# Optimization experiments

Measured on AMD Instinct MI355X. Metric: run time of the kernel, lower is better.

## Reference

```python
import jax, jax.numpy as jnp
import numpy as np

N, E, F_IN, H, C, G, NC = 10000, 160000, 512, 8, 64, 64, 64


def setup_inputs() -> dict:
    key = jax.random.key(0)
    ks = jax.random.split(key, 16)
    d = {}
    d['x'] = jax.random.normal(ks[0], (N, F_IN), jnp.float32)
    d['edge_index'] = jax.random.randint(ks[1], (2, E), 0, N, dtype=jnp.int32)
    d['batch'] = jnp.sort(jax.random.randint(ks[2], (N,), 0, G, dtype=jnp.int32))
    s = 0.05
    d['enc_W'] = jax.random.normal(ks[3], (F_IN, H * C), jnp.float32) * s
    d['enc_b'] = jnp.zeros((H * C,), jnp.float32)
    d['W1'] = jax.random.normal(ks[4], (H * C, H * C), jnp.float32) * s
    d['as1'] = jax.random.normal(ks[5], (H, C), jnp.float32) * s
    d['ad1'] = jax.random.normal(ks[6], (H, C), jnp.float32) * s
    d['b1'] = jnp.zeros((H * C,), jnp.float32)
    d['g1'] = jnp.ones((H * C,), jnp.float32)
    d['be1'] = jnp.zeros((H * C,), jnp.float32)
    d['W2'] = jax.random.normal(ks[7], (H * C, H * C), jnp.float32) * s
    d['as2'] = jax.random.normal(ks[8], (H, C), jnp.float32) * s
    d['ad2'] = jax.random.normal(ks[9], (H, C), jnp.float32) * s
    d['b2'] = jnp.zeros((H * C,), jnp.float32)
    d['g2'] = jnp.ones((H * C,), jnp.float32)
    d['be2'] = jnp.zeros((H * C,), jnp.float32)
    d['W3'] = jax.random.normal(ks[10], (H * C, C), jnp.float32) * s
    d['as3'] = jax.random.normal(ks[11], (1, C), jnp.float32) * s
    d['ad3'] = jax.random.normal(ks[12], (1, C), jnp.float32) * s
    d['b3'] = jnp.zeros((C,), jnp.float32)
    d['g3'] = jnp.ones((C,), jnp.float32)
    d['be3'] = jnp.zeros((C,), jnp.float32)
    d['lin_W'] = jax.random.normal(ks[13], (C, NC), jnp.float32) * s
    d['lin_b'] = jnp.zeros((NC,), jnp.float32)
    return d


def _gat_conv(x, src, dst, W, a_s, a_d, bias, concat):
    # PyG GATConv (eval mode, self-loops already appended to src/dst)
    n = x.shape[0]
    heads, c = a_s.shape
    h = (x @ W).reshape(n, heads, c)                      # [N,H,C]
    logits = (h * a_s).sum(-1)[src] + (h * a_d).sum(-1)[dst]  # [E',H]
    logits = jax.nn.leaky_relu(logits, 0.2)
    m = jax.ops.segment_max(logits, dst, num_segments=n)  # segment softmax over dst
    e = jnp.exp(logits - m[dst])
    s = jax.ops.segment_sum(e, dst, num_segments=n)
    alpha = e / (s[dst] + 1e-16)                          # [E',H]
    out = jax.ops.segment_sum(alpha[:, :, None] * h[src], dst, num_segments=n)
    out = out.reshape(n, heads * c) if concat else out.mean(axis=1)
    return out + bias


def _bn(x, g, b):
    # BatchNorm1d, training-mode statistics (biased var), eps=1e-5
    mu = x.mean(axis=0)
    var = ((x - mu) ** 2).mean(axis=0)
    return g * (x - mu) / jnp.sqrt(var + 1e-5) + b


def reference(x, edge_index, batch, enc_W, enc_b,
              W1, as1, ad1, b1, g1, be1,
              W2, as2, ad2, b2, g2, be2,
              W3, as3, ad3, b3, g3, be3,
              lin_W, lin_b):
    n = x.shape[0]
    loops = jnp.arange(n, dtype=edge_index.dtype)
    src = jnp.concatenate([edge_index[0], loops])
    dst = jnp.concatenate([edge_index[1], loops])
    x = x @ enc_W + enc_b
    # layer 1 (concat heads) + bn + elu + residual
    h = x
    x = _gat_conv(x, src, dst, W1, as1, ad1, b1, True)
    x = jax.nn.elu(_bn(x, g1, be1))
    x = h + x
    # layer 2
    h = x
    x = _gat_conv(x, src, dst, W2, as2, ad2, b2, True)
    x = jax.nn.elu(_bn(x, g2, be2))
    x = h + x
    # layer 3 (heads=1, mean/no-concat), bn, no elu, no residual (shape mismatch)
    x = _gat_conv(x, src, dst, W3, as3, ad3, b3, False)
    x = _bn(x, g3, be3)
    # global mean pool over graphs
    sums = jax.ops.segment_sum(x, batch, num_segments=G)
    cnt = jax.ops.segment_sum(jnp.ones((n,), x.dtype), batch, num_segments=G)
    xg = sums / jnp.clip(cnt, 1.0)[:, None]
    return xg @ lin_W + lin_b
```

## Files before the change

### kernel.cpp

```cpp
#include <hip/hip_runtime.h>
#include <hip/hip_bf16.h>
#include <math.h>

#define NNODES 10000
#define RPAD   10240
#define MPAD   10112
#define EDGES  160000
#define EPLUS  170000
#define FIN    512
#define HEADS8 8
#define CH     64
#define HC     512
#define NG     64
#define NCLS   64
#define NSTAT  256
#define NSTAT3 64

typedef _Float16 f16x8 __attribute__((ext_vector_type(8)));
typedef _Float16 f16x4 __attribute__((ext_vector_type(4)));
typedef _Float16 f16x2 __attribute__((ext_vector_type(2)));
typedef float    f32x4 __attribute__((ext_vector_type(4)));

#define GLD_LDS16(g, l)                                                        \
    __builtin_amdgcn_global_load_lds(                                          \
        (const __attribute__((address_space(1))) void*)(g),                    \
        (__attribute__((address_space(3))) void*)(l), 16, 0, 0)

#define PREP_CNT  665
#define PREP_CONV 5000
__global__ void prep_all(const int* __restrict__ ei, int* __restrict__ deg,
                         const int* __restrict__ batch, int* __restrict__ goff,
                         const float* __restrict__ x_in, _Float16* __restrict__ x16,
                         const float* __restrict__ Wa, const float* __restrict__ Wb,
                         const float* __restrict__ Wc, const float* __restrict__ Wd,
                         _Float16* __restrict__ Ta, _Float16* __restrict__ Tb,
                         _Float16* __restrict__ Tc, _Float16* __restrict__ Td,
                         _Float16* __restrict__ g16pad, float* __restrict__ g3opad)
{
    const int b   = blockIdx.x;
    const int tid = threadIdx.x;
    if (b < PREP_CNT) {
        const float4 z4 = make_float4(0.f, 0.f, 0.f, 0.f);
        if (b < 60)
            ((float4*)g16pad)[b * 256 + tid] = z4;
        else if (b < 75)
            ((float4*)g3opad)[(b - 60) * 256 + tid] = z4;
        int e = b * 256 + tid;
        if (e < NNODES) {
            int bb = batch[e];
            int bprev = (e == 0) ? -1 : batch[e - 1];
            for (int g = bprev + 1; g <= bb; ++g) goff[g] = e;
            if (e == NNODES - 1)
                for (int g = bb + 1; g <= NG; ++g) goff[g] = NNODES;
        }
        if (e >= EPLUS) return;
        int dst = (e < EDGES) ? ei[EDGES + e] : (e - EDGES);
        atomicAdd(&deg[dst], 1);
    } else if (b < PREP_CNT + PREP_CONV) {
        int i = (b - PREP_CNT) * 256 + tid;
        float4 v = ((const float4*)x_in)[i];
        f16x4 o;
        o[0] = (_Float16)v.x; o[1] = (_Float16)v.y;
        o[2] = (_Float16)v.z; o[3] = (_Float16)v.w;
        ((f16x4*)x16)[i] = o;
    } else {
        int tb = b - (PREP_CNT + PREP_CONV);
        int z  = tb >> 8;
        int rem = tb & 255;
        int bxi = rem & 15, byi = rem >> 4;
        if (z == 3 && bxi >= 2) return;
        const float* W = (z == 0) ? Wa : (z == 1) ? Wb : (z == 2) ? Wc : Wd;
        _Float16*    T = (z == 0) ? Ta : (z == 1) ? Tb : (z == 2) ? Tc : Td;
        const int ldW = (z == 3) ? 64 : 512;
        __shared__ float t[32][33];
        int bx = bxi * 32, by = byi * 32;
        int tx = tid & 31, ty = tid >> 5;
        #pragma unroll
        for (int i = 0; i < 32; i += 8)
            t[ty + i][tx] = W[(size_t)(by + ty + i) * ldW + bx + tx];
        __syncthreads();
        #pragma unroll
        for (int i = 0; i < 32; i += 8)
            T[(size_t)(bx + ty + i) * 512 + by + tx] = (_Float16)t[tx][ty + i];
    }
}

__device__ void exscan_dev(const int* __restrict__ deg, int* __restrict__ off,
                           int* __restrict__ cursor, int* partial )
{
    const int tid = threadIdx.x;
    const int chunk = (NNODES + 255) / 256;
    int begin = tid * chunk;
    int end   = begin + chunk; if (end > NNODES) end = NNODES;
    if (begin > NNODES) begin = NNODES;
    int s = 0;
    for (int i = begin; i < end; ++i) s += deg[i];
    partial[tid] = s;
    __syncthreads();
    for (int o = 1; o < 256; o <<= 1) {
        int v = (tid >= o) ? partial[tid - o] : 0;
        __syncthreads();
        partial[tid] += v;
        __syncthreads();
    }
    int run = (tid > 0) ? partial[tid - 1] : 0;
    for (int i = begin; i < end; ++i) {
        off[i] = run; cursor[i] = run; run += deg[i];
    }
    if (tid == 255) off[NNODES] = run;
}

__global__ __launch_bounds__(256) void gemm_f16_mfma(
    const _Float16* __restrict__ A16, const _Float16* __restrict__ Bt16,
    const float* __restrict__ bias, _Float16* __restrict__ C16,
    float* __restrict__ ssrc, float* __restrict__ sdst,
    const float* __restrict__ a_s, const float* __restrict__ a_d,
    int Mt, int Nn, int K,
    int tail, const int* __restrict__ tp0, int* __restrict__ tp1,
    int* __restrict__ tp2)
{
    __shared__ _Float16 As[128 * 32] __attribute__((aligned(16)));
    __shared__ _Float16 Bs[128 * 32] __attribute__((aligned(16)));
    const int tid  = threadIdx.x;
    const int ncols = Nn >> 7;
    const int nb    = ncols * (Mt >> 7);
    const int bid   = blockIdx.x;

    if (bid >= nb) {
        if (tail == 1) {
            exscan_dev(tp0, tp1, tp2, (int*)As);
        } else if (tail == 2) {
            int e = (bid - nb) * 256 + tid;
            if (e < EPLUS) {
                int srcN, dstN;
                if (e < EDGES) { srcN = tp0[e]; dstN = tp0[EDGES + e]; }
                else           { srcN = dstN = e - EDGES; }
                int pos = atomicAdd(&tp1[dstN], 1);
                tp2[pos] = srcN;
            }
        }
        return;
    }

    const int bt   = bid % ncols;
    const int row0 = (bid / ncols) * 128;
    const int col0 = bt * 128;
    const int wave = tid >> 6;
    const int lane = tid & 63;
    const int wy = wave >> 1, wx = wave & 1;

    const int lrow = lane >> 2;
    const int lk   = (lane & 3) * 8;

    f32x4 acc[4][4] = {};

    for (int k0 = 0; k0 < K; k0 += 32) {
        if (k0) __syncthreads();
        #pragma unroll
        for (int r = 0; r < 2; ++r) {
            const int chunk = r * 4 + wave;
            const int trow  = chunk * 16 + lrow;
            GLD_LDS16(A16 + (size_t)(row0 + trow) * K + k0 + lk,
                      &As[chunk * 512]);
            GLD_LDS16(Bt16 + (size_t)(col0 + trow) * K + k0 + lk,
                      &Bs[chunk * 512]);
        }
        __syncthreads();

        const int quad = lane >> 4;
        const int l16  = lane & 15;
        f16x8 af[4], bf[4];
        #pragma unroll
        for (int m = 0; m < 4; ++m)
            af[m] = *(const f16x8*)&As[(wy * 64 + m * 16 + l16) * 32 + quad * 8];
        #pragma unroll
        for (int n = 0; n < 4; ++n)
            bf[n] = *(const f16x8*)&Bs[(wx * 64 + n * 16 + l16) * 32 + quad * 8];
        #pragma unroll
        for (int m = 0; m < 4; ++m)
            #pragma unroll
            for (int n = 0; n < 4; ++n)
                acc[m][n] = __builtin_amdgcn_mfma_f32_16x16x32_f16(
                    af[m], bf[n], acc[m][n], 0, 0, 0);
    }

    const int quad = lane >> 4;
    const int l16  = lane & 15;
    #pragma unroll
    for (int m = 0; m < 4; ++m) {
        #pragma unroll
        for (int n = 0; n < 4; ++n) {
            const int col = col0 + wx * 64 + n * 16 + l16;
            const float bv = bias ? bias[col] : 0.0f;
            #pragma unroll
            for (int r = 0; r < 4; ++r) {
                const int row = row0 + wy * 64 + m * 16 + quad * 4 + r;
                C16[(size_t)row * Nn + col] = (_Float16)(acc[m][n][r] + bv);
            }
        }
    }

    if (ssrc) {
        const int head = bt * 2 + wx;
        float a_sv[4], a_dv[4];
        #pragma unroll
        for (int n = 0; n < 4; ++n) {
            const int col = col0 + wx * 64 + n * 16 + l16;
            a_sv[n] = a_s[col & 511];
            a_dv[n] = a_d[col & 511];
        }
        #pragma unroll
        for (int m = 0; m < 4; ++m) {
            #pragma unroll
            for (int r = 0; r < 4; ++r) {
                float vs = acc[m][0][r] * a_sv[0] + acc[m][1][r] * a_sv[1]
                         + acc[m][2][r] * a_sv[2] + acc[m][3][r] * a_sv[3];
                float vd = acc[m][0][r] * a_dv[0] + acc[m][1][r] * a_dv[1]
                         + acc[m][2][r] * a_dv[2] + acc[m][3][r] * a_dv[3];
                vs += __shfl_xor(vs, 1); vs += __shfl_xor(vs, 2);
                vs += __shfl_xor(vs, 4); vs += __shfl_xor(vs, 8);
                vd += __shfl_xor(vd, 1); vd += __shfl_xor(vd, 2);
                vd += __shfl_xor(vd, 4); vd += __shfl_xor(vd, 8);
                if (l16 == 0) {
                    const int row = row0 + wy * 64 + m * 16 + quad * 4 + r;
                    ssrc[(size_t)row * HEADS8 + head] = vs;
                    sdst[(size_t)row * HEADS8 + head] = vd;
                }
            }
        }
    }
}

__global__ __launch_bounds__(256) void gemm_f16_mfma_n64(
    const _Float16* __restrict__ A16, const _Float16* __restrict__ Bt16,
    _Float16* __restrict__ C16,
    float* __restrict__ ssrc, float* __restrict__ sdst,
    const float* __restrict__ a_s, const float* __restrict__ a_d)
{
    __shared__ _Float16 As[64 * 32] __attribute__((aligned(16)));
    __shared__ _Float16 Bs[64 * 32] __attribute__((aligned(16)));
    __shared__ float sS[2][64];
    __shared__ float sD[2][64];
    const int tid  = threadIdx.x;
    const int wave = tid >> 6;
    const int lane = tid & 63;
    const int row0 = blockIdx.x * 64;
    const int wy = wave >> 1, wx = wave & 1;

    const int lrow = lane >> 2;
    const int lk   = (lane & 3) * 8;

    f32x4 acc[2][2] = {};

    for (int k0 = 0; k0 < 512; k0 += 32) {
        if (k0) __syncthreads();
        {
            const int trow = wave * 16 + lrow;
            GLD_LDS16(A16 + (size_t)(row0 + trow) * 512 + k0 + lk, &As[wave * 512]);
            GLD_LDS16(Bt16 + (size_t)trow * 512 + k0 + lk, &Bs[wave * 512]);
        }
        __syncthreads();

        const int quad = lane >> 4;
        const int l16  = lane & 15;
        f16x8 af[2], bf[2];
        #pragma unroll
        for (int m = 0; m < 2; ++m)
            af[m] = *(const f16x8*)&As[(wy * 32 + m * 16 + l16) * 32 + quad * 8];
        #pragma unroll
        for (int n = 0; n < 2; ++n)
            bf[n] = *(const f16x8*)&Bs[(wx * 32 + n * 16 + l16) * 32 + quad * 8];
        #pragma unroll
        for (int m = 0; m < 2; ++m)
            #pragma unroll
            for (int n = 0; n < 2; ++n)
                acc[m][n] = __builtin_amdgcn_mfma_f32_16x16x32_f16(
                    af[m], bf[n], acc[m][n], 0, 0, 0);
    }

    const int quad = lane >> 4;
    const int l16  = lane & 15;
    #pragma unroll
    for (int m = 0; m < 2; ++m)
        #pragma unroll
        for (int n = 0; n < 2; ++n) {
            const int col = wx * 32 + n * 16 + l16;
            #pragma unroll
            for (int r = 0; r < 4; ++r) {
                const int row = row0 + wy * 32 + m * 16 + quad * 4 + r;
                C16[(size_t)row * 64 + col] = (_Float16)acc[m][n][r];
            }
        }

    {
        float a_sv[2], a_dv[2];
        #pragma unroll
        for (int n = 0; n < 2; ++n) {
            const int col = wx * 32 + n * 16 + l16;
            a_sv[n] = a_s[col];
            a_dv[n] = a_d[col];
        }
        #pragma unroll
        for (int m = 0; m < 2; ++m)
            #pragma unroll
            for (int r = 0; r < 4; ++r) {
                float vs = acc[m][0][r] * a_sv[0] + acc[m][1][r] * a_sv[1];
                float vd = acc[m][0][r] * a_dv[0] + acc[m][1][r] * a_dv[1];
                vs += __shfl_xor(vs, 1); vs += __shfl_xor(vs, 2);
                vs += __shfl_xor(vs, 4); vs += __shfl_xor(vs, 8);
                vd += __shfl_xor(vd, 1); vd += __shfl_xor(vd, 2);
                vd += __shfl_xor(vd, 4); vd += __shfl_xor(vd, 8);
                if (l16 == 0) {
                    const int lr = wy * 32 + m * 16 + quad * 4 + r;
                    sS[wx][lr] = vs;
                    sD[wx][lr] = vd;
                }
            }
        __syncthreads();
        if (wx == 0 && l16 == 0) {
            #pragma unroll
            for (int m = 0; m < 2; ++m)
                #pragma unroll
                for (int r = 0; r < 4; ++r) {
                    const int lr = wy * 32 + m * 16 + quad * 4 + r;
                    const int row = row0 + lr;
                    ssrc[row] = sS[0][lr] + sS[1][lr];
                    sdst[row] = sD[0][lr] + sD[1][lr];
                }
        }
    }
}

__global__ __launch_bounds__(64) void gat_aggregate8(
    const _Float16* __restrict__ Hf, const float* __restrict__ ssrc,
    const float* __restrict__ sdst, const int* __restrict__ off,
    const int* __restrict__ csr, const float* __restrict__ bias,
    _Float16* __restrict__ out)
{
    const int n    = blockIdx.x;
    const int lane = threadIdx.x;
    const int head = lane >> 3;
    const int e0 = off[n], e1 = off[n + 1];

    float4 sd0 = ((const float4*)(sdst + n * 8))[0];
    float4 sd1 = ((const float4*)(sdst + n * 8))[1];
    float sd[8] = {sd0.x, sd0.y, sd0.z, sd0.w, sd1.x, sd1.y, sd1.z, sd1.w};

    __shared__ float exL[64 * 8];
    __shared__ int   srcL[64];
    float acc[8]  = {};
    float ssum[8] = {};
    for (int base = e0; base < e1; base += 64) {
        int cnt = e1 - base; if (cnt > 64) cnt = 64;
        if (lane < cnt) {
            int s = csr[base + lane];
            srcL[lane] = s;
            float4 s0 = ((const float4*)(ssrc + s * 8))[0];
            float4 s1 = ((const float4*)(ssrc + s * 8))[1];
            float lv[8] = {s0.x, s0.y, s0.z, s0.w, s1.x, s1.y, s1.z, s1.w};
            #pragma unroll
            for (int h = 0; h < 8; ++h) {
                float l = lv[h] + sd[h];
                l = (l > 0.f) ? l : 0.2f * l;
                float ex = __expf(l);
                exL[lane * 8 + h] = ex;
                ssum[h] += ex;
            }
        }
        __syncthreads();
        int j = 0;
        for (; j + 8 <= cnt; j += 8) {
            f16x8 hv[8];
            #pragma unroll
            for (int u = 0; u < 8; ++u)
                hv[u] = *(const f16x8*)(Hf + (size_t)srcL[j + u] * HC + lane * 8);
            #pragma unroll
            for (int u = 0; u < 8; ++u) {
                const float a = exL[(j + u) * 8 + head];
                #pragma unroll
                for (int c = 0; c < 8; ++c)
                    acc[c] = fmaf(a, (float)hv[u][c], acc[c]);
            }
        }
        for (; j + 4 <= cnt; j += 4) {
            const int s0 = srcL[j],     s1 = srcL[j + 1];
            const int s2 = srcL[j + 2], s3 = srcL[j + 3];
            f16x8 h0 = *(const f16x8*)(Hf + (size_t)s0 * HC + lane * 8);
            f16x8 h1 = *(const f16x8*)(Hf + (size_t)s1 * HC + lane * 8);
            f16x8 h2 = *(const f16x8*)(Hf + (size_t)s2 * HC + lane * 8);
            f16x8 h3 = *(const f16x8*)(Hf + (size_t)s3 * HC + lane * 8);
            const float a0 = exL[(j)     * 8 + head];
            const float a1 = exL[(j + 1) * 8 + head];
            const float a2 = exL[(j + 2) * 8 + head];
            const float a3 = exL[(j + 3) * 8 + head];
            #pragma unroll
            for (int c = 0; c < 8; ++c) {
                acc[c] = fmaf(a0, (float)h0[c], acc[c]);
                acc[c] = fmaf(a1, (float)h1[c], acc[c]);
                acc[c] = fmaf(a2, (float)h2[c], acc[c]);
                acc[c] = fmaf(a3, (float)h3[c], acc[c]);
            }
        }
        for (; j < cnt; ++j) {
            const int s = srcL[j];
            f16x8 hv = *(const f16x8*)(Hf + (size_t)s * HC + lane * 8);
            const float al = exL[j * 8 + head];
            #pragma unroll
            for (int c = 0; c < 8; ++c)
                acc[c] = fmaf(al, (float)hv[c], acc[c]);
        }
        __syncthreads();
    }
    #pragma unroll
    for (int h = 0; h < 8; ++h)
        #pragma unroll
        for (int o = 1; o < 64; o <<= 1)
            ssum[h] += __shfl_xor(ssum[h], o);

    const float inv = 1.0f / (ssum[head] + 1e-16f);
    const float* bp = bias + lane * 8;
    f16x8 ov;
    #pragma unroll
    for (int c = 0; c < 8; ++c)
        ov[c] = (_Float16)(acc[c] * inv + bp[c]);
    *(f16x8*)(out + (size_t)n * HC + lane * 8) = ov;
}

__global__ __launch_bounds__(64) void gat_aggregate1(
    const _Float16* __restrict__ Hf, const float* __restrict__ ssrc,
    const float* __restrict__ sdst, const int* __restrict__ off,
    const int* __restrict__ csr, const float* __restrict__ bias,
    float* __restrict__ out)
{
    const int n    = blockIdx.x;
    const int lane = threadIdx.x;
    const int e0 = off[n], e1 = off[n + 1];
    const float sd = sdst[n];

    __shared__ float exL[64];
    __shared__ int   srcL[64];
    float acc = 0.f, ssum = 0.f;
    for (int base = e0; base < e1; base += 64) {
        int cnt = e1 - base; if (cnt > 64) cnt = 64;
        if (lane < cnt) {
            int s = csr[base + lane];
            srcL[lane] = s;
            float l = ssrc[s] + sd;
            l = (l > 0.f) ? l : 0.2f * l;
            float ex = __expf(l);
            exL[lane] = ex;
            ssum += ex;
        }
        __syncthreads();
        int j = 0;
        for (; j + 4 <= cnt; j += 4) {
            const int s0 = srcL[j],     s1 = srcL[j + 1];
            const int s2 = srcL[j + 2], s3 = srcL[j + 3];
            float h0 = (float)Hf[(size_t)s0 * 64 + lane];
            float h1 = (float)Hf[(size_t)s1 * 64 + lane];
            float h2 = (float)Hf[(size_t)s2 * 64 + lane];
            float h3 = (float)Hf[(size_t)s3 * 64 + lane];
            acc = fmaf(exL[j],     h0, acc);
            acc = fmaf(exL[j + 1], h1, acc);
            acc = fmaf(exL[j + 2], h2, acc);
            acc = fmaf(exL[j + 3], h3, acc);
        }
        for (; j < cnt; ++j)
            acc = fmaf(exL[j], (float)Hf[(size_t)srcL[j] * 64 + lane], acc);
        __syncthreads();
    }
    #pragma unroll
    for (int o = 1; o < 64; o <<= 1)
        ssum += __shfl_xor(ssum, o);

    out[(size_t)n * 64 + lane] = acc / (ssum + 1e-16f) + bias[lane];
}

__global__ __launch_bounds__(256) void bn_stats_f16(
    const _Float16* __restrict__ x,
    float* __restrict__ psum, float* __restrict__ psq)
{
    const int t    = threadIdx.x;
    const int lane = t & 63;
    const int wv   = t >> 6;
    const int w    = blockIdx.x * 4 + wv;
    float s[8] = {}, q[8] = {};
    #pragma unroll
    for (int k = 0; k < RPAD / 2048; ++k) {
        const int r0 = w + k * 2048;
        f16x8 v0 = *(const f16x8*)(x + (size_t)r0 * HC + lane * 8);
        f16x8 v1 = *(const f16x8*)(x + (size_t)(r0 + 1024) * HC + lane * 8);
        #pragma unroll
        for (int j = 0; j < 8; ++j) {
            float f0 = (float)v0[j], f1 = (float)v1[j];
            s[j] += f0 + f1;
            q[j] += f0 * f0 + f1 * f1;
        }
    }
    __shared__ float ls[4][HC];
    __shared__ float lq[4][HC];
    #pragma unroll
    for (int j = 0; j < 8; ++j) {
        ls[wv][lane * 8 + j] = s[j];
        lq[wv][lane * 8 + j] = q[j];
    }
    __syncthreads();
    const size_t bo = (size_t)blockIdx.x * HC;
    #pragma unroll
    for (int k = 0; k < 2; ++k) {
        const int ch = t + k * 256;
        psum[bo + ch] = ls[0][ch] + ls[1][ch] + ls[2][ch] + ls[3][ch];
        psq [bo + ch] = lq[0][ch] + lq[1][ch] + lq[2][ch] + lq[3][ch];
    }
}

__global__ __launch_bounds__(256) void bn_stats3(
    const float* __restrict__ x,
    float* __restrict__ psum, float* __restrict__ psq)
{
    const int t    = threadIdx.x;
    const int c4   = (t & 15) * 4;
    const int rsub = t >> 4;
    float s[4] = {}, q[4] = {};
    #pragma unroll
    for (int k = 0; k < RPAD / 1024; ++k) {
        const int r = blockIdx.x * 16 + rsub + k * 1024;
        float4 v = *(const float4*)(x + (size_t)r * CH + c4);
        s[0] += v.x; q[0] += v.x * v.x;
        s[1] += v.y; q[1] += v.y * v.y;
        s[2] += v.z; q[2] += v.z * v.z;
        s[3] += v.w; q[3] += v.w * v.w;
    }
    __shared__ float ls[16][CH];
    __shared__ float lq[16][CH];
    #pragma unroll
    for (int j = 0; j < 4; ++j) {
        ls[rsub][c4 + j] = s[j];
        lq[rsub][c4 + j] = q[j];
    }
    __syncthreads();
    if (t < CH) {
        float tot = 0.f;
        #pragma unroll
        for (int p = 0; p < 16; ++p) tot += ls[p][t];
        psum[(size_t)blockIdx.x * CH + t] = tot;
    } else if (t < 2 * CH) {
        const int ch = t - CH;
        float tot = 0.f;
        #pragma unroll
        for (int p = 0; p < 16; ++p) tot += lq[p][ch];
        psq[(size_t)blockIdx.x * CH + ch] = tot;
    }
}

__global__ __launch_bounds__(256) void bn_finalize(
    const float* __restrict__ psum, const float* __restrict__ psq,
    const float* __restrict__ g, const float* __restrict__ be,
    float* __restrict__ scale, float* __restrict__ shift,
    float invN, int cols, int np)
{
    const int t  = threadIdx.x;
    const int pg = t >> 4;
    const int cl = t & 15;
    const int ch = blockIdx.x * 16 + cl;
    float S = 0.f, Q = 0.f;
    for (int p = pg; p < np; p += 16) {
        S += psum[(size_t)p * cols + ch];
        Q += psq [(size_t)p * cols + ch];
    }
    __shared__ float lsS[16][16];
    __shared__ float lsQ[16][16];
    lsS[pg][cl] = S;
    lsQ[pg][cl] = Q;
    __syncthreads();
    if (t < 16) {
        float S2 = 0.f, Q2 = 0.f;
        #pragma unroll
        for (int p = 0; p < 16; ++p) { S2 += lsS[p][t]; Q2 += lsQ[p][t]; }
        const int c = blockIdx.x * 16 + t;
        float mu  = S2 * invN;
        float var = Q2 * invN - mu * mu;
        float sc  = g[c] / sqrtf(var + 1e-5f);
        scale[c] = sc;
        shift[c] = be[c] - mu * sc;
    }
}

__global__ void bn_apply16(const _Float16* __restrict__ xin,
                           const _Float16* __restrict__ res,
                           const float* __restrict__ scale,
                           const float* __restrict__ shift,
                           _Float16* __restrict__ out, size_t total8)
{
    size_t i = (size_t)blockIdx.x * blockDim.x + threadIdx.x;
    if (i >= total8) return;
    int c = (int)((i * 8) & (size_t)(HC - 1));
    f16x8 xv = ((const f16x8*)xin)[i];
    f16x8 rv = ((const f16x8*)res)[i];
    float4 sa = *(const float4*)(scale + c);
    float4 sb = *(const float4*)(scale + c + 4);
    float4 ha = *(const float4*)(shift + c);
    float4 hb = *(const float4*)(shift + c + 4);
    float sc[8] = {sa.x, sa.y, sa.z, sa.w, sb.x, sb.y, sb.z, sb.w};
    float sh[8] = {ha.x, ha.y, ha.z, ha.w, hb.x, hb.y, hb.z, hb.w};
    f16x8 o;
    #pragma unroll
    for (int j = 0; j < 8; ++j) {
        float v = (float)xv[j] * sc[j] + sh[j];
        v = (v > 0.f) ? v : expm1f(v);
        o[j] = (_Float16)(v + (float)rv[j]);
    }
    ((f16x8*)out)[i] = o;
}

__global__ __launch_bounds__(256) void pool_linear(
    const float* __restrict__ x, const int* __restrict__ goff,
    const float* __restrict__ W, const float* __restrict__ b,
    const float* __restrict__ scale, const float* __restrict__ shift,
    float* __restrict__ out)
{
    const int g    = blockIdx.x;
    const int lane = threadIdx.x & 63;
    const int wave = threadIdx.x >> 6;
    const int r0 = goff[g], r1 = goff[g + 1];
    float s = 0.f;
    for (int r = r0 + wave; r < r1; r += 4)
        s += x[(size_t)r * CH + lane];
    __shared__ float red[4][CH];
    __shared__ float mean_l[CH];
    red[wave][lane] = s;
    __syncthreads();
    if (wave == 0) {
        float tot = red[0][lane] + red[1][lane] + red[2][lane] + red[3][lane];
        float cnt = (float)(r1 - r0);
        float m = tot / fmaxf(cnt, 1.0f);
        mean_l[lane] = m * scale[lane] + shift[lane];
    }
    __syncthreads();
    if (threadIdx.x < NCLS) {
        const int j = threadIdx.x;
        float acc = b[j];
        for (int c = 0; c < CH; ++c)
            acc = fmaf(mean_l[c], W[c * NCLS + j], acc);
        out[g * NCLS + j] = acc;
    }
}

extern "C" void kernel_launch(void* const* d_in, const int* in_sizes, int n_in,
                              void* d_out, int out_size, void* d_ws, size_t ws_size,
                              hipStream_t stream)
{
    const float* x_in  = (const float*)d_in[0];
    const int*   ei    = (const int*)  d_in[1];
    const int*   batch = (const int*)  d_in[2];
    const float* enc_W = (const float*)d_in[3];
    const float* enc_b = (const float*)d_in[4];
    const float* W1  = (const float*)d_in[5];
    const float* as1 = (const float*)d_in[6];
    const float* ad1 = (const float*)d_in[7];
    const float* b1  = (const float*)d_in[8];
    const float* g1  = (const float*)d_in[9];
    const float* be1 = (const float*)d_in[10];
    const float* W2  = (const float*)d_in[11];
    const float* as2 = (const float*)d_in[12];
    const float* ad2 = (const float*)d_in[13];
    const float* b2  = (const float*)d_in[14];
    const float* g2  = (const float*)d_in[15];
    const float* be2 = (const float*)d_in[16];
    const float* W3  = (const float*)d_in[17];
    const float* as3 = (const float*)d_in[18];
    const float* ad3 = (const float*)d_in[19];
    const float* b3  = (const float*)d_in[20];
    const float* g3  = (const float*)d_in[21];
    const float* be3 = (const float*)d_in[22];
    const float* linW = (const float*)d_in[23];
    const float* linb = (const float*)d_in[24];
    float* out = (float*)d_out;

    char* ws = (char*)d_ws;
    size_t off_b = 0;
    auto alloc = [&](size_t bytes) -> void* {
        void* p = ws + off_b;
        off_b = (off_b + bytes + 255) & ~(size_t)255;
        return p;
    };
    _Float16* f16A   = (_Float16*)alloc((size_t)MPAD * HC * 2);
    _Float16* f16B   = (_Float16*)alloc((size_t)MPAD * HC * 2);
    _Float16* H16    = (_Float16*)alloc((size_t)MPAD * HC * 2);
    _Float16* g16    = (_Float16*)alloc((size_t)RPAD * HC * 2);
    _Float16* h3_16  = (_Float16*)alloc((size_t)MPAD * CH * 2);
    float*    g3o    = (float*)alloc((size_t)RPAD * CH * 4);
    _Float16* encWt  = (_Float16*)alloc((size_t)HC * FIN * 2);
    _Float16* W1t    = (_Float16*)alloc((size_t)HC * HC * 2);
    _Float16* W2t    = (_Float16*)alloc((size_t)HC * HC * 2);
    _Float16* W3t    = (_Float16*)alloc((size_t)CH * HC * 2);
    float* ssrc   = (float*)alloc((size_t)MPAD * HEADS8 * 4);
    float* sdst   = (float*)alloc((size_t)MPAD * HEADS8 * 4);
    int*   deg    = (int*)  alloc((size_t)NNODES * 4);
    int*   offp   = (int*)  alloc((size_t)(NNODES + 1) * 4);
    int*   cursor = (int*)  alloc((size_t)NNODES * 4);
    int*   csr    = (int*)  alloc((size_t)EPLUS * 4);
    int*   goff   = (int*)  alloc((size_t)(NG + 1) * 4);
    float* psum   = (float*)alloc((size_t)NSTAT * HC * 4);
    float* psq    = (float*)alloc((size_t)NSTAT * HC * 4);
    float* psum3  = (float*)alloc((size_t)NSTAT3 * CH * 4);
    float* psq3   = (float*)alloc((size_t)NSTAT3 * CH * 4);
    float* bnsc   = (float*)alloc(HC * 4);
    float* bnsh   = (float*)alloc(HC * 4);

    hipMemsetAsync(deg, 0, (size_t)NNODES * 4, stream);
    prep_all<<<PREP_CNT + PREP_CONV + 1024, 256, 0, stream>>>(
        ei, deg, batch, goff, x_in, f16A, enc_W, W1, W2, W3,
        encWt, W1t, W2t, W3t,
        g16 + (size_t)NNODES * HC, g3o + (size_t)NNODES * CH);

    const int NB = (HC / 128) * (MPAD / 128);
    const int SCAT = (EPLUS + 255) / 256;

    gemm_f16_mfma<<<NB + 1, 256, 0, stream>>>(
        f16A, encWt, enc_b, f16B, nullptr, nullptr, nullptr, nullptr,
        MPAD, HC, FIN, 1, deg, offp, cursor);

    const size_t total8 = (size_t)NNODES * HC / 8;
    const int apply_blocks = (int)((total8 + 255) / 256);
    const float invN = 1.0f / NNODES;

    gemm_f16_mfma<<<NB + SCAT, 256, 0, stream>>>(
        f16B, W1t, nullptr, H16, ssrc, sdst, as1, ad1,
        MPAD, HC, HC, 2, ei, cursor, csr);
    gat_aggregate8<<<NNODES, 64, 0, stream>>>(H16, ssrc, sdst, offp, csr,
                                              b1, g16);
    bn_stats_f16<<<NSTAT, 256, 0, stream>>>(g16, psum, psq);
    bn_finalize<<<HC / 16, 256, 0, stream>>>(psum, psq, g1, be1, bnsc, bnsh,
                                             invN, HC, NSTAT);
    bn_apply16<<<apply_blocks, 256, 0, stream>>>(g16, f16B, bnsc, bnsh,
                                                 f16A, total8);

    gemm_f16_mfma<<<NB, 256, 0, stream>>>(
        f16A, W2t, nullptr, H16, ssrc, sdst, as2, ad2,
        MPAD, HC, HC, 0, nullptr, nullptr, nullptr);
    gat_aggregate8<<<NNODES, 64, 0, stream>>>(H16, ssrc, sdst, offp, csr,
                                              b2, g16);
    bn_stats_f16<<<NSTAT, 256, 0, stream>>>(g16, psum, psq);
    bn_finalize<<<HC / 16, 256, 0, stream>>>(psum, psq, g2, be2, bnsc, bnsh,
                                             invN, HC, NSTAT);
    bn_apply16<<<apply_blocks, 256, 0, stream>>>(g16, f16A, bnsc, bnsh,
                                                 f16B, total8);

    gemm_f16_mfma_n64<<<MPAD / 64, 256, 0, stream>>>(f16B, W3t, h3_16,
                                                     ssrc, sdst, as3, ad3);
    gat_aggregate1<<<NNODES, 64, 0, stream>>>(h3_16, ssrc, sdst, offp, csr,
                                              b3, g3o);
    bn_stats3<<<NSTAT3, 256, 0, stream>>>(g3o, psum3, psq3);
    bn_finalize<<<CH / 16, 256, 0, stream>>>(psum3, psq3, g3, be3, bnsc, bnsh,
                                             invN, CH, NSTAT3);

    pool_linear<<<NG, 256, 0, stream>>>(g3o, goff, linW, linb, bnsc, bnsh,
                                        out);
}
```

Before: 313.5 us.

## Pack four nodes per aggregate block, remap GEMM blocks per XCD, fuse final BN

The aggregation kernels now run four independent waves per 256-thread block, each handling one node with its own LDS slice. Block barriers become wave barriers, and far fewer blocks are launched. The GEMM remaps block IDs so that consecutive tiles land on the same XCD, aiming for better L2 locality. The layer-3 BN finalize is folded into pool_linear, which removes one launch but makes each of the 64 pool blocks redundantly reduce the partial statistics.

Result: no change. 315.8 us (+0.8%).

```diff
diff --git a/kernel.cpp b/kernel.cpp
--- a/kernel.cpp
+++ b/kernel.cpp
@@ -15,6 +15,7 @@
 #define NCLS   64
 #define NSTAT  256
 #define NSTAT3 64
+#define AGG_BLKS 2500
 
 typedef _Float16 f16x8 __attribute__((ext_vector_type(8)));
 typedef _Float16 f16x4 __attribute__((ext_vector_type(4)));
@@ -124,7 +125,7 @@
     const int tid  = threadIdx.x;
     const int ncols = Nn >> 7;
     const int nb    = ncols * (Mt >> 7);
-    const int bid   = blockIdx.x;
+    int bid = blockIdx.x;
 
     if (bid >= nb) {
         if (tail == 1) {
@@ -140,6 +141,12 @@
             }
         }
         return;
+    }
+
+    {
+        const int q = nb >> 3, r = nb & 7;
+        const int xcd = bid & 7, pos = bid >> 3;
+        bid = (xcd < r ? xcd * (q + 1) : r * (q + 1) + (xcd - r) * q) + pos;
     }
 
     const int bt   = bid % ncols;
@@ -331,30 +338,34 @@
     }
 }
 
-__global__ __launch_bounds__(64) void gat_aggregate8(
+__global__ __launch_bounds__(256) void gat_aggregate8(
     const _Float16* __restrict__ Hf, const float* __restrict__ ssrc,
     const float* __restrict__ sdst, const int* __restrict__ off,
     const int* __restrict__ csr, const float* __restrict__ bias,
     _Float16* __restrict__ out)
 {
-    const int n    = blockIdx.x;
-    const int lane = threadIdx.x;
+    const int wv   = threadIdx.x >> 6;
+    const int lane = threadIdx.x & 63;
     const int head = lane >> 3;
+    const int n    = blockIdx.x * 4 + wv;
+
+    __shared__ float exL[4][512];
+    __shared__ int   srcL[4][64];
+    float* exW  = exL[wv];
+    int*   srcW = srcL[wv];
+
     const int e0 = off[n], e1 = off[n + 1];
-
     float4 sd0 = ((const float4*)(sdst + n * 8))[0];
     float4 sd1 = ((const float4*)(sdst + n * 8))[1];
     float sd[8] = {sd0.x, sd0.y, sd0.z, sd0.w, sd1.x, sd1.y, sd1.z, sd1.w};
 
-    __shared__ float exL[64 * 8];
-    __shared__ int   srcL[64];
     float acc[8]  = {};
     float ssum[8] = {};
     for (int base = e0; base < e1; base += 64) {
         int cnt = e1 - base; if (cnt > 64) cnt = 64;
         if (lane < cnt) {
             int s = csr[base + lane];
-            srcL[lane] = s;
+            srcW[lane] = s;
             float4 s0 = ((const float4*)(ssrc + s * 8))[0];
             float4 s1 = ((const float4*)(ssrc + s * 8))[1];
             float lv[8] = {s0.x, s0.y, s0.z, s0.w, s1.x, s1.y, s1.z, s1.w};
@@ -363,36 +374,36 @@
                 float l = lv[h] + sd[h];
                 l = (l > 0.f) ? l : 0.2f * l;
                 float ex = __expf(l);
-                exL[lane * 8 + h] = ex;
+                exW[lane * 8 + h] = ex;
                 ssum[h] += ex;
             }
         }
-        __syncthreads();
+        __builtin_amdgcn_wave_barrier();
         int j = 0;
         for (; j + 8 <= cnt; j += 8) {
             f16x8 hv[8];
             #pragma unroll
             for (int u = 0; u < 8; ++u)
-                hv[u] = *(const f16x8*)(Hf + (size_t)srcL[j + u] * HC + lane * 8);
+                hv[u] = *(const f16x8*)(Hf + (size_t)srcW[j + u] * HC + lane * 8);
             #pragma unroll
             for (int u = 0; u < 8; ++u) {
-                const float a = exL[(j + u) * 8 + head];
+                const float a = exW[(j + u) * 8 + head];
                 #pragma unroll
                 for (int c = 0; c < 8; ++c)
                     acc[c] = fmaf(a, (float)hv[u][c], acc[c]);
             }
         }
         for (; j + 4 <= cnt; j += 4) {
-            const int s0 = srcL[j],     s1 = srcL[j + 1];
-            const int s2 = srcL[j + 2], s3 = srcL[j + 3];
+            const int s0 = srcW[j],     s1 = srcW[j + 1];
+            const int s2 = srcW[j + 2], s3 = srcW[j + 3];
             f16x8 h0 = *(const f16x8*)(Hf + (size_t)s0 * HC + lane * 8);
             f16x8 h1 = *(const f16x8*)(Hf + (size_t)s1 * HC + lane * 8);
             f16x8 h2 = *(const f16x8*)(Hf + (size_t)s2 * HC + lane * 8);
             f16x8 h3 = *(const f16x8*)(Hf + (size_t)s3 * HC + lane * 8);
-            const float a0 = exL[(j)     * 8 + head];
-            const float a1 = exL[(j + 1) * 8 + head];
-            const float a2 = exL[(j + 2) * 8 + head];
-            const float a3 = exL[(j + 3) * 8 + head];
+            const float a0 = exW[(j)     * 8 + head];
+            const float a1 = exW[(j + 1) * 8 + head];
+            const float a2 = exW[(j + 2) * 8 + head];
+            const float a3 = exW[(j + 3) * 8 + head];
             #pragma unroll
             for (int c = 0; c < 8; ++c) {
                 acc[c] = fmaf(a0, (float)h0[c], acc[c]);
@@ -402,14 +413,14 @@
             }
         }
         for (; j < cnt; ++j) {
-            const int s = srcL[j];
+            const int s = srcW[j];
             f16x8 hv = *(const f16x8*)(Hf + (size_t)s * HC + lane * 8);
-            const float al = exL[j * 8 + head];
+            const float al = exW[j * 8 + head];
             #pragma unroll
             for (int c = 0; c < 8; ++c)
                 acc[c] = fmaf(al, (float)hv[c], acc[c]);
         }
-        __syncthreads();
+        __builtin_amdgcn_wave_barrier();
     }
     #pragma unroll
     for (int h = 0; h < 8; ++h)
@@ -426,48 +437,53 @@
     *(f16x8*)(out + (size_t)n * HC + lane * 8) = ov;
 }
 
-__global__ __launch_bounds__(64) void gat_aggregate1(
+__global__ __launch_bounds__(256) void gat_aggregate1(
     const _Float16* __restrict__ Hf, const float* __restrict__ ssrc,
     const float* __restrict__ sdst, const int* __restrict__ off,
     const int* __restrict__ csr, const float* __restrict__ bias,
     float* __restrict__ out)
 {
-    const int n    = blockIdx.x;
-    const int lane = threadIdx.x;
+    const int wv   = threadIdx.x >> 6;
+    const int lane = threadIdx.x & 63;
+    const int n    = blockIdx.x * 4 + wv;
+
+    __shared__ float exL[4][64];
+    __shared__ int   srcL[4][64];
+    float* exW  = exL[wv];
+    int*   srcW = srcL[wv];
+
     const int e0 = off[n], e1 = off[n + 1];
     const float sd = sdst[n];
 
-    __shared__ float exL[64];
-    __shared__ int   srcL[64];
     float acc = 0.f, ssum = 0.f;
     for (int base = e0; base < e1; base += 64) {
         int cnt = e1 - base; if (cnt > 64) cnt = 64;
         if (lane < cnt) {
             int s = csr[base + lane];
-            srcL[lane] = s;
+            srcW[lane] = s;
             float l = ssrc[s] + sd;
             l = (l > 0.f) ? l : 0.2f * l;
             float ex = __expf(l);
-            exL[lane] = ex;
+            exW[lane] = ex;
             ssum += ex;
         }
-        __syncthreads();
+        __builtin_amdgcn_wave_barrier();
         int j = 0;
         for (; j + 4 <= cnt; j += 4) {
-            const int s0 = srcL[j],     s1 = srcL[j + 1];
-            const int s2 = srcL[j + 2], s3 = srcL[j + 3];
+            const int s0 = srcW[j],     s1 = srcW[j + 1];
+            const int s2 = srcW[j + 2], s3 = srcW[j + 3];
             float h0 = (float)Hf[(size_t)s0 * 64 + lane];
             float h1 = (float)Hf[(size_t)s1 * 64 + lane];
             float h2 = (float)Hf[(size_t)s2 * 64 + lane];
             float h3 = (float)Hf[(size_t)s3 * 64 + lane];
-            acc = fmaf(exL[j],     h0, acc);
-            acc = fmaf(exL[j + 1], h1, acc);
-            acc = fmaf(exL[j + 2], h2, acc);
-            acc = fmaf(exL[j + 3], h3, acc);
+            acc = fmaf(exW[j],     h0, acc);
+            acc = fmaf(exW[j + 1], h1, acc);
+            acc = fmaf(exW[j + 2], h2, acc);
+            acc = fmaf(exW[j + 3], h3, acc);
         }
         for (; j < cnt; ++j)
-            acc = fmaf(exL[j], (float)Hf[(size_t)srcL[j] * 64 + lane], acc);
-        __syncthreads();
+            acc = fmaf(exW[j], (float)Hf[(size_t)srcW[j] * 64 + lane], acc);
+        __builtin_amdgcn_wave_barrier();
     }
     #pragma unroll
     for (int o = 1; o < 64; o <<= 1)
@@ -616,25 +632,43 @@
 __global__ __launch_bounds__(256) void pool_linear(
     const float* __restrict__ x, const int* __restrict__ goff,
     const float* __restrict__ W, const float* __restrict__ b,
-    const float* __restrict__ scale, const float* __restrict__ shift,
-    float* __restrict__ out)
+    const float* __restrict__ psum3, const float* __restrict__ psq3,
+    const float* __restrict__ g3, const float* __restrict__ be3,
+    float invN, float* __restrict__ out)
 {
     const int g    = blockIdx.x;
     const int lane = threadIdx.x & 63;
     const int wave = threadIdx.x >> 6;
+    __shared__ float fS[4][CH];
+    __shared__ float fQ[4][CH];
+    __shared__ float red[4][CH];
+    __shared__ float mean_l[CH];
+    {
+        float S = 0.f, Q = 0.f;
+        for (int p = wave; p < NSTAT3; p += 4) {
+            S += psum3[(size_t)p * CH + lane];
+            Q += psq3 [(size_t)p * CH + lane];
+        }
+        fS[wave][lane] = S;
+        fQ[wave][lane] = Q;
+    }
     const int r0 = goff[g], r1 = goff[g + 1];
     float s = 0.f;
     for (int r = r0 + wave; r < r1; r += 4)
         s += x[(size_t)r * CH + lane];
-    __shared__ float red[4][CH];
-    __shared__ float mean_l[CH];
     red[wave][lane] = s;
     __syncthreads();
     if (wave == 0) {
         float tot = red[0][lane] + red[1][lane] + red[2][lane] + red[3][lane];
+        float S = fS[0][lane] + fS[1][lane] + fS[2][lane] + fS[3][lane];
+        float Q = fQ[0][lane] + fQ[1][lane] + fQ[2][lane] + fQ[3][lane];
+        float mu  = S * invN;
+        float var = Q * invN - mu * mu;
+        float sc  = g3[lane] / sqrtf(var + 1e-5f);
+        float sh  = be3[lane] - mu * sc;
         float cnt = (float)(r1 - r0);
         float m = tot / fmaxf(cnt, 1.0f);
-        mean_l[lane] = m * scale[lane] + shift[lane];
+        mean_l[lane] = m * sc + sh;
     }
     __syncthreads();
     if (threadIdx.x < NCLS) {
@@ -728,8 +762,8 @@
     gemm_f16_mfma<<<NB + SCAT, 256, 0, stream>>>(
         f16B, W1t, nullptr, H16, ssrc, sdst, as1, ad1,
         MPAD, HC, HC, 2, ei, cursor, csr);
-    gat_aggregate8<<<NNODES, 64, 0, stream>>>(H16, ssrc, sdst, offp, csr,
-                                              b1, g16);
+    gat_aggregate8<<<AGG_BLKS, 256, 0, stream>>>(H16, ssrc, sdst, offp, csr,
+                                                 b1, g16);
     bn_stats_f16<<<NSTAT, 256, 0, stream>>>(g16, psum, psq);
     bn_finalize<<<HC / 16, 256, 0, stream>>>(psum, psq, g1, be1, bnsc, bnsh,
                                              invN, HC, NSTAT);
@@ -739,8 +773,8 @@
     gemm_f16_mfma<<<NB, 256, 0, stream>>>(
         f16A, W2t, nullptr, H16, ssrc, sdst, as2, ad2,
         MPAD, HC, HC, 0, nullptr, nullptr, nullptr);
-    gat_aggregate8<<<NNODES, 64, 0, stream>>>(H16, ssrc, sdst, offp, csr,
-                                              b2, g16);
+    gat_aggregate8<<<AGG_BLKS, 256, 0, stream>>>(H16, ssrc, sdst, offp, csr,
+                                                 b2, g16);
     bn_stats_f16<<<NSTAT, 256, 0, stream>>>(g16, psum, psq);
     bn_finalize<<<HC / 16, 256, 0, stream>>>(psum, psq, g2, be2, bnsc, bnsh,
                                              invN, HC, NSTAT);
@@ -749,12 +783,10 @@
 
     gemm_f16_mfma_n64<<<MPAD / 64, 256, 0, stream>>>(f16B, W3t, h3_16,
                                                      ssrc, sdst, as3, ad3);
-    gat_aggregate1<<<NNODES, 64, 0, stream>>>(h3_16, ssrc, sdst, offp, csr,
-                                              b3, g3o);
+    gat_aggregate1<<<AGG_BLKS, 256, 0, stream>>>(h3_16, ssrc, sdst, offp, csr,
+                                                 b3, g3o);
     bn_stats3<<<NSTAT3, 256, 0, stream>>>(g3o, psum3, psq3);
-    bn_finalize<<<CH / 16, 256, 0, stream>>>(psum3, psq3, g3, be3, bnsc, bnsh,
-                                             invN, CH, NSTAT3);
-
-    pool_linear<<<NG, 256, 0, stream>>>(g3o, goff, linW, linb, bnsc, bnsh,
-                                        out);
-}
+
+    pool_linear<<<NG, 256, 0, stream>>>(g3o, goff, linW, linb,
+                                        psum3, psq3, g3, be3, invN, out);
+}
```
